# Performance work log

Measured on AMD Instinct MI355X. Metric: run time of the kernel, lower is better.

The kernel has to match this reference:

```python
import jax, jax.numpy as jnp
import numpy as np

VOCAB, D, SLOTS, K = 50257, 512, 16, 3
B, T_FULL = 64, 2049
EPS_LN = 1e-5


def setup_inputs() -> dict:
    key = jax.random.key(0)
    ks = jax.random.split(key, 12)
    u = jax.random.uniform(ks[0], (B, T_FULL - 1), jnp.float32)
    gumbel = -jnp.log(-jnp.log(u + 1e-8) + 1e-8)
    s = 0.02
    return {
        "seq": jax.random.randint(ks[1], (B, T_FULL), 0, VOCAB),
        "temperature": jnp.ones((), jnp.float32),
        "gumbel": gumbel,
        "embed": jax.random.normal(ks[2], (VOCAB, D), jnp.float32) * s,
        "W1": jax.random.normal(ks[3], (D, 2 * D), jnp.float32) * s,
        "b1": jnp.zeros((2 * D,), jnp.float32),
        "W2": jax.random.normal(ks[4], (2 * D, D), jnp.float32) * s,
        "b2": jnp.zeros((D,), jnp.float32),
        "gamma": jnp.ones((D,), jnp.float32),
        "beta": jnp.zeros((D,), jnp.float32),
        "Wg": jax.random.normal(ks[5], (D,), jnp.float32) * s,
        "bg": jnp.zeros((), jnp.float32),
        "Wr": jax.random.normal(ks[6], (D, D), jnp.float32) * s,
        "br": jnp.zeros((D,), jnp.float32),
        "Wo": jax.random.normal(ks[7], (D, VOCAB), jnp.float32) * s,
        "bo": jnp.zeros((VOCAB,), jnp.float32),
    }


def reference(seq, temperature, gumbel, embed, W1, b1, W2, b2, gamma, beta, Wg, bg, Wr, br, Wo, bo):
    # Encoder: embed -> FFN residual -> LayerNorm
    h = embed[seq]                                        # [B, T+1, D]
    ff = jnp.maximum(h @ W1 + b1, 0.0) @ W2 + b2
    x = h + ff
    mu = jnp.mean(x, -1, keepdims=True)
    var = jnp.mean((x - mu) ** 2, -1, keepdims=True)
    hiddens = (x - mu) * jax.lax.rsqrt(var + EPS_LN) * gamma + beta

    context = hiddens[:, :-1, :]                          # [B, T, D]
    gate = context @ Wg + bg                              # [B, T]

    # gumbel top-k with straight-through mask (forward value = hard mask)
    perturbed = (gate + gumbel) / temperature
    _, idx = jax.lax.top_k(perturbed, K)                  # [B, K]
    mask = jnp.zeros_like(gate).at[jnp.arange(B)[:, None], idx].set(1.0)
    soft = jax.nn.softmax(perturbed, axis=-1)
    sel = mask + soft - jax.lax.stop_gradient(soft)

    # gather selected hidden states, scatter_add into memory slots
    gw = jnp.take_along_axis(sel, idx, axis=1)            # [B, K]
    gh = jnp.take_along_axis(context, idx[..., None], axis=1)  # [B, K, D]
    weighted = gh * gw[..., None]
    slot_idx = jnp.arange(K) % SLOTS
    mem = jnp.zeros((B, SLOTS, D), hiddens.dtype).at[:, slot_idx, :].add(weighted)

    # attention read with last-position query
    q = hiddens[:, -1, :] @ Wr + br                       # [B, D]
    scores = jnp.einsum('bsd,bd->bs', mem, q)
    attn = jax.nn.softmax(scores, axis=-1)
    ctx = jnp.einsum('bs,bsd->bd', attn, mem)
    return ctx @ Wo + bo                                  # [B, vocab]
```

## Files before the change

kernel.cpp:

```cpp
#include <hip/hip_runtime.h>
#include <math.h>

#define TFULL 2049
#define TCTX  2048
#define Vm    50257

typedef __attribute__((ext_vector_type(8))) short bf16x8;
typedef __attribute__((ext_vector_type(4))) float f32x4;

__device__ __forceinline__ float wred64(float v){
  #pragma unroll
  for (int m = 1; m < 64; m <<= 1) v += __shfl_xor(v, m, 64);
  return v;
}
__device__ __forceinline__ short bf16_rn(float x){
  union { float f; unsigned u; } c; c.f = x;
  unsigned r = c.u + 0x7fff + ((c.u >> 16) & 1);
  return (short)(r >> 16);
}
__device__ __forceinline__ float bf16_f(short s){
  union { float f; unsigned u; } c; c.u = ((unsigned)(unsigned short)s) << 16;
  return c.f;
}

#define FMA4(ACC_, S_, W_)                         \
  (ACC_).x = fmaf((S_), (W_).x, (ACC_).x);         \
  (ACC_).y = fmaf((S_), (W_).y, (ACC_).y);         \
  (ACC_).z = fmaf((S_), (W_).z, (ACC_).z);         \
  (ACC_).w = fmaf((S_), (W_).w, (ACC_).w);

__global__ void k0_setup(const float* __restrict__ gamma, const float* __restrict__ beta,
                         const float* __restrict__ Wg, float* __restrict__ scal){
  const int t = threadIdx.x;
  float wg = Wg[t];
  float g  = gamma[t]*wg, bw = beta[t]*wg;
  scal[2 + t] = g;
  g = wred64(g); bw = wred64(bw);
  __shared__ float ra[8], rb[8];
  if ((t & 63) == 0){ ra[t>>6] = g; rb[t>>6] = bw; }
  __syncthreads();
  if (t == 0){
    float G = 0.f, Bw = 0.f;
    #pragma unroll
    for (int i = 0; i < 8; ++i){ G += ra[i]; Bw += rb[i]; }
    scal[0] = G; scal[1] = Bw;
  }
}

__global__ __launch_bounds__(256) void kpack(const float* __restrict__ W, int N, int KB,
                                             short* __restrict__ hi, short* __restrict__ lo){
  int i = blockIdx.x*256 + threadIdx.x;
  if (i >= KB*N*4) return;
  int kq = i & 3;
  int n  = (i >> 2) % N;
  int kb = i / (N*4);
  const float* src = W + (kb*32 + kq*8)*N + n;
  bf16x8 h8, l8;
  #pragma unroll
  for (int j = 0; j < 8; ++j){
    float w = src[j*N];
    short h = bf16_rn(w);
    h8[j] = h;
    l8[j] = bf16_rn(w - bf16_f(h));
  }
  *(bf16x8*)(hi + i*8) = h8;
  *(bf16x8*)(lo + i*8) = l8;
}

__global__ __launch_bounds__(512, 2) void k1_main(
    const int*   __restrict__ seq,   const float* __restrict__ temp,
    const float* __restrict__ gumbel,const float* __restrict__ embed,
    const short* __restrict__ W1h,   const short* __restrict__ W1l,
    const float* __restrict__ b1,
    const short* __restrict__ W2h,   const short* __restrict__ W2l,
    const float* __restrict__ b2,
    const float* __restrict__ gamma, const float* __restrict__ beta,
    const float* __restrict__ bg,
    const float* __restrict__ scal,
    float* __restrict__ pert, float* __restrict__ qh)
{
  __shared__ short Ah[16*1280];
  __shared__ short Al[16*1280];
  __shared__ short Rh[8*1024];
  __shared__ short Rl[8*1024];
  __shared__ float Xq[512];
  __shared__ int   srow[32];
  __shared__ float redS1[256], redS2[256], redSG[256];
  __shared__ float redMu[32], redRs[32];

  const int t    = threadIdx.x;
  const int tile = blockIdx.x;
  const int lane = t & 63;
  const int wv   = t >> 6;
  const int mrow = lane & 15;
  const int kq   = lane >> 4;
  const int crow0 = kq*4;

  if (t < 32) srow[t] = seq[tile*32 + t];
  __syncthreads();

  const f32x4* __restrict__ embv = (const f32x4*)embed;
  #pragma unroll
  for (int k = 0; k < 8; ++k){
    int f4  = k*512 + t;
    int tok = f4 >> 7, c4 = f4 & 127;
    f32x4 v = __builtin_nontemporal_load(embv + srow[tok]*128 + c4);
    int d0 = c4*4;
    int base = (d0>>5)*1280 + tok*40 + ((d0>>3)&3)*8 + (d0&7);
    short h0 = bf16_rn(v[0]), h1 = bf16_rn(v[1]), h2 = bf16_rn(v[2]), h3 = bf16_rn(v[3]);
    Ah[base+0] = h0; Ah[base+1] = h1; Ah[base+2] = h2; Ah[base+3] = h3;
    Al[base+0] = bf16_rn(v[0] - bf16_f(h0));
    Al[base+1] = bf16_rn(v[1] - bf16_f(h1));
    Al[base+2] = bf16_rn(v[2] - bf16_f(h2));
    Al[base+3] = bf16_rn(v[3] - bf16_f(h3));
  }
  __syncthreads();

  f32x4 ff[4][2];
  #pragma unroll
  for (int i = 0; i < 4; ++i){
    ff[i][0] = (f32x4){0.f,0.f,0.f,0.f};
    ff[i][1] = (f32x4){0.f,0.f,0.f,0.f};
  }

  for (int ch = 0; ch < 4; ++ch){
    f32x4 acc[2][2];
    #pragma unroll
    for (int i = 0; i < 2; ++i){
      acc[i][0] = (f32x4){0.f,0.f,0.f,0.f};
      acc[i][1] = (f32x4){0.f,0.f,0.f,0.f};
    }
    #pragma unroll 2
    for (int kb = 0; kb < 16; ++kb){
      bf16x8 ah0 = *(const bf16x8*)(Ah + kb*1280 + mrow*40 + kq*8);
      bf16x8 al0 = *(const bf16x8*)(Al + kb*1280 + mrow*40 + kq*8);
      bf16x8 ah1 = *(const bf16x8*)(Ah + kb*1280 + (mrow+16)*40 + kq*8);
      bf16x8 al1 = *(const bf16x8*)(Al + kb*1280 + (mrow+16)*40 + kq*8);
      #pragma unroll
      for (int nt = 0; nt < 2; ++nt){
        int n = ch*256 + wv*32 + nt*16 + mrow;
        int off = (((kb<<10) + n)*4 + kq)*8;
        bf16x8 bh = *(const bf16x8*)(W1h + off);
        bf16x8 bl = *(const bf16x8*)(W1l + off);
        acc[nt][0] = __builtin_amdgcn_mfma_f32_16x16x32_bf16(ah0, bh, acc[nt][0], 0,0,0);
        acc[nt][0] = __builtin_amdgcn_mfma_f32_16x16x32_bf16(al0, bh, acc[nt][0], 0,0,0);
        acc[nt][0] = __builtin_amdgcn_mfma_f32_16x16x32_bf16(ah0, bl, acc[nt][0], 0,0,0);
        acc[nt][1] = __builtin_amdgcn_mfma_f32_16x16x32_bf16(ah1, bh, acc[nt][1], 0,0,0);
        acc[nt][1] = __builtin_amdgcn_mfma_f32_16x16x32_bf16(al1, bh, acc[nt][1], 0,0,0);
        acc[nt][1] = __builtin_amdgcn_mfma_f32_16x16x32_bf16(ah1, bl, acc[nt][1], 0,0,0);
      }
    }
    __syncthreads();
    #pragma unroll
    for (int nt = 0; nt < 2; ++nt){
      int jcol = wv*32 + nt*16 + mrow;
      float bb = b1[ch*256 + jcol];
      int rbase = (jcol>>5)*1024 + ((jcol>>3)&3)*8 + (jcol&7);
      #pragma unroll
      for (int mt = 0; mt < 2; ++mt){
        #pragma unroll
        for (int r = 0; r < 4; ++r){
          int tok = mt*16 + crow0 + r;
          float a = fmaxf(acc[nt][mt][r] + bb, 0.f);
          short h = bf16_rn(a);
          Rh[rbase + tok*32] = h;
          Rl[rbase + tok*32] = bf16_rn(a - bf16_f(h));
        }
      }
    }
    __syncthreads();
    #pragma unroll 2
    for (int kb = 0; kb < 8; ++kb){
      bf16x8 ah0 = *(const bf16x8*)(Rh + kb*1024 + mrow*32 + kq*8);
      bf16x8 al0 = *(const bf16x8*)(Rl + kb*1024 + mrow*32 + kq*8);
      bf16x8 ah1 = *(const bf16x8*)(Rh + kb*1024 + (mrow+16)*32 + kq*8);
      bf16x8 al1 = *(const bf16x8*)(Rl + kb*1024 + (mrow+16)*32 + kq*8);
      int kbg = ch*8 + kb;
      #pragma unroll
      for (int nt = 0; nt < 4; ++nt){
        int n = wv*64 + nt*16 + mrow;
        int off = (((kbg<<9) + n)*4 + kq)*8;
        bf16x8 bh = *(const bf16x8*)(W2h + off);
        bf16x8 bl = *(const bf16x8*)(W2l + off);
        ff[nt][0] = __builtin_amdgcn_mfma_f32_16x16x32_bf16(ah0, bh, ff[nt][0], 0,0,0);
        ff[nt][0] = __builtin_amdgcn_mfma_f32_16x16x32_bf16(al0, bh, ff[nt][0], 0,0,0);
        ff[nt][0] = __builtin_amdgcn_mfma_f32_16x16x32_bf16(ah0, bl, ff[nt][0], 0,0,0);
        ff[nt][1] = __builtin_amdgcn_mfma_f32_16x16x32_bf16(ah1, bh, ff[nt][1], 0,0,0);
        ff[nt][1] = __builtin_amdgcn_mfma_f32_16x16x32_bf16(al1, bh, ff[nt][1], 0,0,0);
        ff[nt][1] = __builtin_amdgcn_mfma_f32_16x16x32_bf16(ah1, bl, ff[nt][1], 0,0,0);
      }
    }
  }

  const float G1 = scal[0], BW = scal[1];
  const float* gWg = scal + 2;
  const float bgv  = bg[0];
  const float invT = 1.0f / temp[0];
  int rem  = (tile*32) % 2049;
  int qtok = 2048 - rem;

  float ps1[2][4], ps2[2][4], psg[2][4];
  #pragma unroll
  for (int mt = 0; mt < 2; ++mt)
    #pragma unroll
    for (int r = 0; r < 4; ++r){ ps1[mt][r]=0.f; ps2[mt][r]=0.f; psg[mt][r]=0.f; }

  #pragma unroll
  for (int nt = 0; nt < 4; ++nt){
    int d = wv*64 + nt*16 + mrow;
    float b2v = b2[d];
    float gw  = gWg[d];
    int abase = (d>>5)*1280 + ((d>>3)&3)*8 + (d&7);
    #pragma unroll
    for (int mt = 0; mt < 2; ++mt){
      #pragma unroll
      for (int r = 0; r < 4; ++r){
        int tok = mt*16 + crow0 + r;
        float h = bf16_f(Ah[abase + tok*40]) + bf16_f(Al[abase + tok*40]);
        float x = h + ff[nt][mt][r] + b2v;
        ps1[mt][r] += x;
        ps2[mt][r] = fmaf(x, x, ps2[mt][r]);
        psg[mt][r] = fmaf(x, gw, psg[mt][r]);
        if (tok == qtok) Xq[d] = x;
      }
    }
  }
  #pragma unroll
  for (int mt = 0; mt < 2; ++mt){
    #pragma unroll
    for (int r = 0; r < 4; ++r){
      float a = ps1[mt][r], b = ps2[mt][r], c = psg[mt][r];
      #pragma unroll
      for (int m = 1; m < 16; m <<= 1){
        a += __shfl_xor(a, m, 64);
        b += __shfl_xor(b, m, 64);
        c += __shfl_xor(c, m, 64);
      }
      if (mrow == 0){
        int tok = mt*16 + crow0 + r;
        redS1[tok*8 + wv] = a;
        redS2[tok*8 + wv] = b;
        redSG[tok*8 + wv] = c;
      }
    }
  }
  __syncthreads();

  if (t < 32){
    float S1 = 0.f, S2 = 0.f, SG = 0.f;
    #pragma unroll
    for (int w = 0; w < 8; ++w){
      S1 += redS1[t*8 + w];
      S2 += redS2[t*8 + w];
      SG += redSG[t*8 + w];
    }
    float mu  = S1 * (1.f/512.f);
    float var = S2 * (1.f/512.f) - mu*mu;
    float rs  = rsqrtf(var + 1e-5f);
    redMu[t] = mu; redRs[t] = rs;
    int id  = tile*32 + t;
    int b   = id / 2049;
    int pos = id - b*2049;
    if (pos < TCTX){
      float gate = rs*(SG - mu*G1) + BW + bgv;
      float pv = (gate + __builtin_nontemporal_load(gumbel + b*TCTX + pos)) * invT;
      __builtin_nontemporal_store(pv, pert + b*TCTX + pos);
    }
  }
  __syncthreads();

  if (qtok < 32 && t < 256){
    int id = tile*32 + qtok;
    int b  = id / 2049;
    float mu = redMu[qtok], rs = redRs[qtok];
    int d = t*2;
    qh[b*512 + d]     = (Xq[d]  -mu)*rs*gamma[d]   + beta[d];
    qh[b*512 + d + 1] = (Xq[d+1]-mu)*rs*gamma[d+1] + beta[d+1];
  }
}

__global__ __launch_bounds__(256) void k2_topk(const float* __restrict__ pert,
                                               int* __restrict__ idxw){
  __shared__ float v[2048];
  __shared__ float wvv[256];
  __shared__ int   wii[256];
  const int b = blockIdx.x, t = threadIdx.x;
  for (int i = t; i < 2048; i += 256) v[i] = pert[b*TCTX + i];
  __syncthreads();
  for (int r = 0; r < 3; ++r){
    float best = -INFINITY; int bi = 1<<30;
    for (int i = t; i < 2048; i += 256){
      float x = v[i];
      if (x > best || (x == best && i < bi)){ best = x; bi = i; }
    }
    wvv[t] = best; wii[t] = bi;
    __syncthreads();
    for (int s = 128; s > 0; s >>= 1){
      if (t < s){
        float ov = wvv[t+s]; int oi = wii[t+s];
        if (ov > wvv[t] || (ov == wvv[t] && oi < wii[t])){ wvv[t] = ov; wii[t] = oi; }
      }
      __syncthreads();
    }
    if (t == 0){ idxw[b*3 + r] = wii[0]; v[wii[0]] = -INFINITY; }
    __syncthreads();
  }
}

__global__ __launch_bounds__(256) void k3_rows(const int* __restrict__ seq,
    const float* __restrict__ embed, const float* __restrict__ W1, const float* __restrict__ b1,
    const float* __restrict__ W2,    const float* __restrict__ b2,
    const float* __restrict__ gamma, const float* __restrict__ beta,
    const int* __restrict__ idxw, float* __restrict__ memr)
{
  __shared__ float hs[512];
  __shared__ float rbuf[1024];
  __shared__ float red1[4], red2[4];
  const int t   = threadIdx.x;
  const int blk = blockIdx.x;
  const int b = blk / 3, kk = blk - b*3;
  const int pos = idxw[b*3 + kk];
  const int row = seq[b*TFULL + pos];
  ((float2*)hs)[t] = ((const float2*)(embed + row*512))[t];
  __syncthreads();
  const float4* W1v = (const float4*)W1;
  float4 a = make_float4(0,0,0,0);
  #pragma unroll 4
  for (int d = 0; d < 512; ++d){
    float xb = hs[d];
    float4 wq = W1v[d*256 + t];
    FMA4(a, xb, wq);
  }
  float4 bq = ((const float4*)b1)[t];
  float4 r;
  r.x = fmaxf(a.x+bq.x, 0.f); r.y = fmaxf(a.y+bq.y, 0.f);
  r.z = fmaxf(a.z+bq.z, 0.f); r.w = fmaxf(a.w+bq.w, 0.f);
  ((float4*)rbuf)[t] = r;
  __syncthreads();
  const float2* W2v2 = (const float2*)W2;
  float fx = 0.f, fy = 0.f;
  #pragma unroll 4
  for (int j = 0; j < 1024; ++j){
    float rb = rbuf[j];
    float2 wq = W2v2[j*256 + t];
    fx = fmaf(rb, wq.x, fx); fy = fmaf(rb, wq.y, fy);
  }
  float2 b2q = ((const float2*)b2)[t];
  float2 hx  = ((float2*)hs)[t];
  float x0 = hx.x + fx + b2q.x;
  float x1 = hx.y + fy + b2q.y;
  float s1 = wred64(x0 + x1);
  float s2 = wred64(x0*x0 + x1*x1);
  if ((t & 63) == 0){ red1[t>>6] = s1; red2[t>>6] = s2; }
  __syncthreads();
  float S1 = red1[0]+red1[1]+red1[2]+red1[3];
  float S2 = red2[0]+red2[1]+red2[2]+red2[3];
  float mu  = S1*(1.f/512.f);
  float var = S2*(1.f/512.f) - mu*mu;
  float rs  = rsqrtf(var + 1e-5f);
  const int dd = t*2;
  memr[(b*3+kk)*512 + dd]     = (x0-mu)*rs*gamma[dd]   + beta[dd];
  memr[(b*3+kk)*512 + dd + 1] = (x1-mu)*rs*gamma[dd+1] + beta[dd+1];
}

__global__ __launch_bounds__(256) void k4_attn(const float* __restrict__ qh,
    const float* __restrict__ Wr, const float* __restrict__ br,
    const float* __restrict__ memr, float* __restrict__ ctxT)
{
  __shared__ float hq[512];
  __shared__ float red[12];
  const int t = threadIdx.x, b = blockIdx.x;
  ((float2*)hq)[t] = ((const float2*)(qh + b*512))[t];
  __syncthreads();
  const float2* Wrv = (const float2*)Wr;
  float qx = 0.f, qy = 0.f;
  #pragma unroll 4
  for (int d = 0; d < 512; ++d){
    float hb = hq[d];
    float2 wq = Wrv[d*256 + t];
    qx = fmaf(hb, wq.x, qx); qy = fmaf(hb, wq.y, qy);
  }
  float2 brq = ((const float2*)br)[t];
  qx += brq.x; qy += brq.y;
  const int dd = t*2;
  const float* m0 = memr + (b*3+0)*512;
  const float* m1 = memr + (b*3+1)*512;
  const float* m2 = memr + (b*3+2)*512;
  float p0 = wred64(qx*m0[dd] + qy*m0[dd+1]);
  float p1 = wred64(qx*m1[dd] + qy*m1[dd+1]);
  float p2 = wred64(qx*m2[dd] + qy*m2[dd+1]);
  if ((t & 63) == 0){ int w = t>>6; red[w*3+0]=p0; red[w*3+1]=p1; red[w*3+2]=p2; }
  __syncthreads();
  float s0 = red[0]+red[3]+red[6]+red[9];
  float s1 = red[1]+red[4]+red[7]+red[10];
  float s2 = red[2]+red[5]+red[8]+red[11];
  float m  = fmaxf(fmaxf(s0, s1), fmaxf(s2, 0.f));
  float e0 = expf(s0-m), e1 = expf(s1-m), e2 = expf(s2-m);
  float den = e0 + e1 + e2 + 13.f*expf(-m);
  float a0 = e0/den, a1 = e1/den, a2 = e2/den;
  float c0 = a0*m0[dd]   + a1*m1[dd]   + a2*m2[dd];
  float c1 = a0*m0[dd+1] + a1*m1[dd+1] + a2*m2[dd+1];
  ctxT[dd*64 + b]     = c0;
  ctxT[(dd+1)*64 + b] = c1;
}

__global__ __launch_bounds__(256) void k5_out(const float* __restrict__ ctxT,
    const float* __restrict__ Wo, const float* __restrict__ bo,
    float* __restrict__ out)
{
  const int v  = blockIdx.x*256 + threadIdx.x;
  const int vc = v < Vm ? v : Vm-1;
  float acc[64];
  #pragma unroll
  for (int b = 0; b < 64; ++b) acc[b] = 0.f;
  for (int d = 0; d < 512; ++d){
    float w = Wo[d*Vm + vc];
    const float* c = ctxT + d*64;
    #pragma unroll
    for (int b = 0; b < 64; ++b) acc[b] = fmaf(c[b], w, acc[b]);
  }
  if (v < Vm){
    float bb = bo[v];
    #pragma unroll
    for (int b = 0; b < 64; ++b) out[b*Vm + v] = acc[b] + bb;
  }
}

extern "C" void kernel_launch(void* const* d_in, const int* in_sizes, int n_in,
                              void* d_out, int out_size, void* d_ws, size_t ws_size,
                              hipStream_t stream){
  (void)in_sizes; (void)n_in; (void)out_size; (void)ws_size;
  const int*   seq   = (const int*)d_in[0];
  const float* temp  = (const float*)d_in[1];
  const float* gum   = (const float*)d_in[2];
  const float* embed = (const float*)d_in[3];
  const float* W1    = (const float*)d_in[4];
  const float* b1    = (const float*)d_in[5];
  const float* W2    = (const float*)d_in[6];
  const float* b2    = (const float*)d_in[7];
  const float* gamma = (const float*)d_in[8];
  const float* beta  = (const float*)d_in[9];
  const float* Wg    = (const float*)d_in[10];
  const float* bg    = (const float*)d_in[11];
  const float* Wr    = (const float*)d_in[12];
  const float* br    = (const float*)d_in[13];
  const float* Wo    = (const float*)d_in[14];
  const float* bo    = (const float*)d_in[15];
  float* out = (float*)d_out;

  float* wsf  = (float*)d_ws;
  float* pert = wsf;
  float* qh   = wsf + 131072;
  float* memr = wsf + 163840;
  float* ctxT = wsf + 262144;
  float* scal = wsf + 294912;
  int*   idxw = (int*)(wsf + 295936);
  short* W1h  = (short*)(wsf + 296192);
  short* W1l  = W1h + 512*1024;
  short* W2h  = W1l + 512*1024;
  short* W2l  = W2h + 1024*512;

  k0_setup<<<1, 512, 0, stream>>>(gamma, beta, Wg, scal);
  kpack<<<256, 256, 0, stream>>>(W1, 1024, 16, W1h, W1l);
  kpack<<<256, 256, 0, stream>>>(W2, 512, 32, W2h, W2l);
  k1_main<<<4098, 512, 0, stream>>>(seq, temp, gum, embed, W1h, W1l, b1,
                                    W2h, W2l, b2, gamma, beta, bg, scal, pert, qh);
  k2_topk<<<64, 256, 0, stream>>>(pert, idxw);
  k3_rows<<<192, 256, 0, stream>>>(seq, embed, W1, b1, W2, b2, gamma, beta, idxw, memr);
  k4_attn<<<64, 256, 0, stream>>>(qh, Wr, br, memr, ctxT);
  k5_out<<<197, 256, 0, stream>>>(ctxT, Wo, bo, out);
}
```

Before: 2.156 ms.

## Double token tile to 64 per block with K-split embedding staging

The main encoder kernel now processes 64 tokens per block instead of 32, halving the grid. Each block therefore reads the packed W1/W2 hi/lo weights once per 64 tokens rather than per 32, cutting weight traffic per token. To fit LDS, the embedding tile is staged in two K-halves and re-gathered from global memory for every FFN chunk. The residual for the first half of the features is recomputed into a reused buffer at the end. The cost is much larger LDS use, likely limiting residency to one block per CU, plus repeated embedding gathers and bf16 splitting.

```diff
diff --git a/kernel.cpp b/kernel.cpp
--- a/kernel.cpp
+++ b/kernel.cpp
@@ -79,14 +79,16 @@
     const float* __restrict__ scal,
     float* __restrict__ pert, float* __restrict__ qh)
 {
-  __shared__ short Ah[16*1280];
-  __shared__ short Al[16*1280];
-  __shared__ short Rh[8*1024];
-  __shared__ short Rl[8*1024];
+  __shared__ short Ah[8*2560];
+  __shared__ short Al[8*2560];
+  __shared__ short Rbuf[32768];
   __shared__ float Xq[512];
-  __shared__ int   srow[32];
-  __shared__ float redS1[256], redS2[256], redSG[256];
-  __shared__ float redMu[32], redRs[32];
+  __shared__ int   srow[64];
+  __shared__ float redS1[512], redS2[512], redSG[512];
+  __shared__ float redMu[64], redRs[64];
+
+  short* Rh = Rbuf;
+  short* Rl = Rbuf + 16384;
 
   const int t    = threadIdx.x;
   const int tile = blockIdx.x;
@@ -96,68 +98,83 @@
   const int kq   = lane >> 4;
   const int crow0 = kq*4;
 
-  if (t < 32) srow[t] = seq[tile*32 + t];
+  if (t < 64) srow[t] = seq[tile*64 + t];
   __syncthreads();
 
   const f32x4* __restrict__ embv = (const f32x4*)embed;
-  #pragma unroll
-  for (int k = 0; k < 8; ++k){
-    int f4  = k*512 + t;
-    int tok = f4 >> 7, c4 = f4 & 127;
-    f32x4 v = __builtin_nontemporal_load(embv + srow[tok]*128 + c4);
-    int d0 = c4*4;
-    int base = (d0>>5)*1280 + tok*40 + ((d0>>3)&3)*8 + (d0&7);
-    short h0 = bf16_rn(v[0]), h1 = bf16_rn(v[1]), h2 = bf16_rn(v[2]), h3 = bf16_rn(v[3]);
-    Ah[base+0] = h0; Ah[base+1] = h1; Ah[base+2] = h2; Ah[base+3] = h3;
-    Al[base+0] = bf16_rn(v[0] - bf16_f(h0));
-    Al[base+1] = bf16_rn(v[1] - bf16_f(h1));
-    Al[base+2] = bf16_rn(v[2] - bf16_f(h2));
-    Al[base+3] = bf16_rn(v[3] - bf16_f(h3));
-  }
-  __syncthreads();
-
-  f32x4 ff[4][2];
-  #pragma unroll
-  for (int i = 0; i < 4; ++i){
-    ff[i][0] = (f32x4){0.f,0.f,0.f,0.f};
-    ff[i][1] = (f32x4){0.f,0.f,0.f,0.f};
-  }
+
+  auto stageA = [&](int hh){
+    #pragma unroll
+    for (int k = 0; k < 8; ++k){
+      int idx = k*512 + t;
+      int tok = idx >> 6, c4 = idx & 63;
+      f32x4 v = __builtin_nontemporal_load(embv + srow[tok]*128 + hh*64 + c4);
+      int dl = c4*4;
+      int base = (dl>>5)*2560 + tok*40 + ((dl>>3)&3)*8 + (dl&7);
+      short h0 = bf16_rn(v[0]), h1 = bf16_rn(v[1]), h2 = bf16_rn(v[2]), h3 = bf16_rn(v[3]);
+      Ah[base+0] = h0; Ah[base+1] = h1; Ah[base+2] = h2; Ah[base+3] = h3;
+      Al[base+0] = bf16_rn(v[0] - bf16_f(h0));
+      Al[base+1] = bf16_rn(v[1] - bf16_f(h1));
+      Al[base+2] = bf16_rn(v[2] - bf16_f(h2));
+      Al[base+3] = bf16_rn(v[3] - bf16_f(h3));
+    }
+  };
+
+  f32x4 ff[4][4];
+  #pragma unroll
+  for (int i = 0; i < 4; ++i)
+    #pragma unroll
+    for (int j = 0; j < 4; ++j) ff[i][j] = (f32x4){0.f,0.f,0.f,0.f};
 
   for (int ch = 0; ch < 4; ++ch){
-    f32x4 acc[2][2];
-    #pragma unroll
-    for (int i = 0; i < 2; ++i){
-      acc[i][0] = (f32x4){0.f,0.f,0.f,0.f};
-      acc[i][1] = (f32x4){0.f,0.f,0.f,0.f};
-    }
-    #pragma unroll 2
-    for (int kb = 0; kb < 16; ++kb){
-      bf16x8 ah0 = *(const bf16x8*)(Ah + kb*1280 + mrow*40 + kq*8);
-      bf16x8 al0 = *(const bf16x8*)(Al + kb*1280 + mrow*40 + kq*8);
-      bf16x8 ah1 = *(const bf16x8*)(Ah + kb*1280 + (mrow+16)*40 + kq*8);
-      bf16x8 al1 = *(const bf16x8*)(Al + kb*1280 + (mrow+16)*40 + kq*8);
-      #pragma unroll
-      for (int nt = 0; nt < 2; ++nt){
-        int n = ch*256 + wv*32 + nt*16 + mrow;
-        int off = (((kb<<10) + n)*4 + kq)*8;
-        bf16x8 bh = *(const bf16x8*)(W1h + off);
-        bf16x8 bl = *(const bf16x8*)(W1l + off);
-        acc[nt][0] = __builtin_amdgcn_mfma_f32_16x16x32_bf16(ah0, bh, acc[nt][0], 0,0,0);
-        acc[nt][0] = __builtin_amdgcn_mfma_f32_16x16x32_bf16(al0, bh, acc[nt][0], 0,0,0);
-        acc[nt][0] = __builtin_amdgcn_mfma_f32_16x16x32_bf16(ah0, bl, acc[nt][0], 0,0,0);
-        acc[nt][1] = __builtin_amdgcn_mfma_f32_16x16x32_bf16(ah1, bh, acc[nt][1], 0,0,0);
-        acc[nt][1] = __builtin_amdgcn_mfma_f32_16x16x32_bf16(al1, bh, acc[nt][1], 0,0,0);
-        acc[nt][1] = __builtin_amdgcn_mfma_f32_16x16x32_bf16(ah1, bl, acc[nt][1], 0,0,0);
-      }
-    }
-    __syncthreads();
+    f32x4 acc[2][4];
+    #pragma unroll
+    for (int i = 0; i < 2; ++i)
+      #pragma unroll
+      for (int j = 0; j < 4; ++j) acc[i][j] = (f32x4){0.f,0.f,0.f,0.f};
+
+    auto g1 = [&](int hh){
+      #pragma unroll 4
+      for (int kbr = 0; kbr < 8; ++kbr){
+        bf16x8 ah[4], al[4];
+        #pragma unroll
+        for (int mt = 0; mt < 4; ++mt){
+          ah[mt] = *(const bf16x8*)(Ah + kbr*2560 + (mrow + 16*mt)*40 + kq*8);
+          al[mt] = *(const bf16x8*)(Al + kbr*2560 + (mrow + 16*mt)*40 + kq*8);
+        }
+        int kbg = hh*8 + kbr;
+        #pragma unroll
+        for (int nt = 0; nt < 2; ++nt){
+          int n = ch*256 + wv*32 + nt*16 + mrow;
+          int off = ((kbg*1024 + n)*4 + kq)*8;
+          bf16x8 bh = *(const bf16x8*)(W1h + off);
+          bf16x8 bl = *(const bf16x8*)(W1l + off);
+          #pragma unroll
+          for (int mt = 0; mt < 4; ++mt){
+            acc[nt][mt] = __builtin_amdgcn_mfma_f32_16x16x32_bf16(ah[mt], bh, acc[nt][mt], 0,0,0);
+            acc[nt][mt] = __builtin_amdgcn_mfma_f32_16x16x32_bf16(al[mt], bh, acc[nt][mt], 0,0,0);
+            acc[nt][mt] = __builtin_amdgcn_mfma_f32_16x16x32_bf16(ah[mt], bl, acc[nt][mt], 0,0,0);
+          }
+        }
+      }
+    };
+
+    stageA(0);
+    __syncthreads();
+    g1(0);
+    __syncthreads();
+    stageA(1);
+    __syncthreads();
+    g1(1);
+    __syncthreads();
+
     #pragma unroll
     for (int nt = 0; nt < 2; ++nt){
       int jcol = wv*32 + nt*16 + mrow;
       float bb = b1[ch*256 + jcol];
-      int rbase = (jcol>>5)*1024 + ((jcol>>3)&3)*8 + (jcol&7);
-      #pragma unroll
-      for (int mt = 0; mt < 2; ++mt){
+      int rbase = (jcol>>5)*2048 + ((jcol>>3)&3)*8 + (jcol&7);
+      #pragma unroll
+      for (int mt = 0; mt < 4; ++mt){
         #pragma unroll
         for (int r = 0; r < 4; ++r){
           int tok = mt*16 + crow0 + r;
@@ -169,39 +186,59 @@
       }
     }
     __syncthreads();
+
     #pragma unroll 2
     for (int kb = 0; kb < 8; ++kb){
-      bf16x8 ah0 = *(const bf16x8*)(Rh + kb*1024 + mrow*32 + kq*8);
-      bf16x8 al0 = *(const bf16x8*)(Rl + kb*1024 + mrow*32 + kq*8);
-      bf16x8 ah1 = *(const bf16x8*)(Rh + kb*1024 + (mrow+16)*32 + kq*8);
-      bf16x8 al1 = *(const bf16x8*)(Rl + kb*1024 + (mrow+16)*32 + kq*8);
+      bf16x8 rh[4], rl[4];
+      #pragma unroll
+      for (int mt = 0; mt < 4; ++mt){
+        rh[mt] = *(const bf16x8*)(Rh + kb*2048 + (mrow + 16*mt)*32 + kq*8);
+        rl[mt] = *(const bf16x8*)(Rl + kb*2048 + (mrow + 16*mt)*32 + kq*8);
+      }
       int kbg = ch*8 + kb;
       #pragma unroll
       for (int nt = 0; nt < 4; ++nt){
         int n = wv*64 + nt*16 + mrow;
-        int off = (((kbg<<9) + n)*4 + kq)*8;
+        int off = ((kbg*512 + n)*4 + kq)*8;
         bf16x8 bh = *(const bf16x8*)(W2h + off);
         bf16x8 bl = *(const bf16x8*)(W2l + off);
-        ff[nt][0] = __builtin_amdgcn_mfma_f32_16x16x32_bf16(ah0, bh, ff[nt][0], 0,0,0);
-        ff[nt][0] = __builtin_amdgcn_mfma_f32_16x16x32_bf16(al0, bh, ff[nt][0], 0,0,0);
-        ff[nt][0] = __builtin_amdgcn_mfma_f32_16x16x32_bf16(ah0, bl, ff[nt][0], 0,0,0);
-        ff[nt][1] = __builtin_amdgcn_mfma_f32_16x16x32_bf16(ah1, bh, ff[nt][1], 0,0,0);
-        ff[nt][1] = __builtin_amdgcn_mfma_f32_16x16x32_bf16(al1, bh, ff[nt][1], 0,0,0);
-        ff[nt][1] = __builtin_amdgcn_mfma_f32_16x16x32_bf16(ah1, bl, ff[nt][1], 0,0,0);
-      }
-    }
-  }
+        #pragma unroll
+        for (int mt = 0; mt < 4; ++mt){
+          ff[nt][mt] = __builtin_amdgcn_mfma_f32_16x16x32_bf16(rh[mt], bh, ff[nt][mt], 0,0,0);
+          ff[nt][mt] = __builtin_amdgcn_mfma_f32_16x16x32_bf16(rl[mt], bh, ff[nt][mt], 0,0,0);
+          ff[nt][mt] = __builtin_amdgcn_mfma_f32_16x16x32_bf16(rh[mt], bl, ff[nt][mt], 0,0,0);
+        }
+      }
+    }
+  }
+
+  __syncthreads();
+  float* hbuf = (float*)Rbuf;
+  #pragma unroll
+  for (int k = 0; k < 8; ++k){
+    int idx = k*512 + t;
+    int tok = idx >> 6, c4 = idx & 63;
+    f32x4 v = __builtin_nontemporal_load(embv + srow[tok]*128 + c4);
+    f32x4 hv;
+    #pragma unroll
+    for (int j = 0; j < 4; ++j){
+      short hi = bf16_rn(v[j]);
+      hv[j] = bf16_f(hi) + bf16_f(bf16_rn(v[j] - bf16_f(hi)));
+    }
+    *(f32x4*)(hbuf + tok*256 + c4*4) = hv;
+  }
+  __syncthreads();
 
   const float G1 = scal[0], BW = scal[1];
   const float* gWg = scal + 2;
   const float bgv  = bg[0];
   const float invT = 1.0f / temp[0];
-  int rem  = (tile*32) % 2049;
+  int rem  = (tile*64) % 2049;
   int qtok = 2048 - rem;
 
-  float ps1[2][4], ps2[2][4], psg[2][4];
-  #pragma unroll
-  for (int mt = 0; mt < 2; ++mt)
+  float ps1[4][4], ps2[4][4], psg[4][4];
+  #pragma unroll
+  for (int mt = 0; mt < 4; ++mt)
     #pragma unroll
     for (int r = 0; r < 4; ++r){ ps1[mt][r]=0.f; ps2[mt][r]=0.f; psg[mt][r]=0.f; }
 
@@ -210,23 +247,39 @@
     int d = wv*64 + nt*16 + mrow;
     float b2v = b2[d];
     float gw  = gWg[d];
-    int abase = (d>>5)*1280 + ((d>>3)&3)*8 + (d&7);
-    #pragma unroll
-    for (int mt = 0; mt < 2; ++mt){
-      #pragma unroll
-      for (int r = 0; r < 4; ++r){
-        int tok = mt*16 + crow0 + r;
-        float h = bf16_f(Ah[abase + tok*40]) + bf16_f(Al[abase + tok*40]);
-        float x = h + ff[nt][mt][r] + b2v;
-        ps1[mt][r] += x;
-        ps2[mt][r] = fmaf(x, x, ps2[mt][r]);
-        psg[mt][r] = fmaf(x, gw, psg[mt][r]);
-        if (tok == qtok) Xq[d] = x;
-      }
-    }
-  }
-  #pragma unroll
-  for (int mt = 0; mt < 2; ++mt){
+    if (wv >= 4){
+      int abase = ((d - 256)>>5)*2560 + ((d>>3)&3)*8 + (d&7);
+      #pragma unroll
+      for (int mt = 0; mt < 4; ++mt){
+        #pragma unroll
+        for (int r = 0; r < 4; ++r){
+          int tok = mt*16 + crow0 + r;
+          float h = bf16_f(Ah[abase + tok*40]) + bf16_f(Al[abase + tok*40]);
+          float x = h + ff[nt][mt][r] + b2v;
+          ps1[mt][r] += x;
+          ps2[mt][r] = fmaf(x, x, ps2[mt][r]);
+          psg[mt][r] = fmaf(x, gw, psg[mt][r]);
+          if (tok == qtok) Xq[d] = x;
+        }
+      }
+    } else {
+      #pragma unroll
+      for (int mt = 0; mt < 4; ++mt){
+        #pragma unroll
+        for (int r = 0; r < 4; ++r){
+          int tok = mt*16 + crow0 + r;
+          float h = hbuf[tok*256 + d];
+          float x = h + ff[nt][mt][r] + b2v;
+          ps1[mt][r] += x;
+          ps2[mt][r] = fmaf(x, x, ps2[mt][r]);
+          psg[mt][r] = fmaf(x, gw, psg[mt][r]);
+          if (tok == qtok) Xq[d] = x;
+        }
+      }
+    }
+  }
+  #pragma unroll
+  for (int mt = 0; mt < 4; ++mt){
     #pragma unroll
     for (int r = 0; r < 4; ++r){
       float a = ps1[mt][r], b = ps2[mt][r], c = psg[mt][r];
@@ -246,7 +299,7 @@
   }
   __syncthreads();
 
-  if (t < 32){
+  if (t < 64){
     float S1 = 0.f, S2 = 0.f, SG = 0.f;
     #pragma unroll
     for (int w = 0; w < 8; ++w){
@@ -258,7 +311,7 @@
     float var = S2 * (1.f/512.f) - mu*mu;
     float rs  = rsqrtf(var + 1e-5f);
     redMu[t] = mu; redRs[t] = rs;
-    int id  = tile*32 + t;
+    int id  = tile*64 + t;
     int b   = id / 2049;
     int pos = id - b*2049;
     if (pos < TCTX){
@@ -269,8 +322,8 @@
   }
   __syncthreads();
 
-  if (qtok < 32 && t < 256){
-    int id = tile*32 + qtok;
+  if (qtok < 64 && t < 256){
+    int id = tile*64 + qtok;
     int b  = id / 2049;
     float mu = redMu[qtok], rs = redRs[qtok];
     int d = t*2;
@@ -463,7 +516,7 @@
   k0_setup<<<1, 512, 0, stream>>>(gamma, beta, Wg, scal);
   kpack<<<256, 256, 0, stream>>>(W1, 1024, 16, W1h, W1l);
   kpack<<<256, 256, 0, stream>>>(W2, 512, 32, W2h, W2l);
-  k1_main<<<4098, 512, 0, stream>>>(seq, temp, gum, embed, W1h, W1l, b1,
+  k1_main<<<2049, 512, 0, stream>>>(seq, temp, gum, embed, W1h, W1l, b1,
                                     W2h, W2l, b2, gamma, beta, bg, scal, pert, qh);
   k2_topk<<<64, 256, 0, stream>>>(pert, idxw);
   k3_rows<<<192, 256, 0, stream>>>(seq, embed, W1, b1, W2, b2, gamma, beta, idxw, memr);
```

Result: slower. 2.226 ms (+3.3%).
